# Kernel optimization log

Measured on AMD Instinct MI355X. Metric: run time of the kernel, lower is better.

The kernel has to match this reference:

```python
import jax, jax.numpy as jnp
import numpy as np

N_TRACKS = 2_000_000
N_EVENTS = 100_000
N_FEAT = 32
N_LATENT = 64


def setup_inputs() -> dict:
    key = jax.random.key(0)
    ks = jax.random.split(key, 12)
    x = jax.random.normal(ks[0], (N_TRACKS, N_FEAT), dtype=jnp.float32)
    # sorted event ids; guarantee every event id 0..N_EVENTS-1 appears so the
    # compacted segment count is exactly N_EVENTS (static shape under jit)
    extra = jax.random.randint(ks[1], (N_TRACKS - N_EVENTS,), 0, N_EVENTS)
    event_ids = jnp.sort(jnp.concatenate([jnp.arange(N_EVENTS), extra])).astype(jnp.int64)

    def lin(k, fan_in, fan_out):
        return jax.random.normal(k, (fan_in, fan_out), dtype=jnp.float32) / np.sqrt(fan_in)

    return {
        "x": x,
        "event_ids": event_ids,
        "phi_w1": lin(ks[2], N_FEAT, 2 * N_FEAT),
        "phi_b1": jnp.zeros((2 * N_FEAT,), jnp.float32),
        "phi_w2": lin(ks[3], 2 * N_FEAT, N_LATENT),
        "phi_b2": jnp.zeros((N_LATENT,), jnp.float32),
        "rho_w1": lin(ks[4], N_LATENT, 2 * N_LATENT),
        "rho_b1": jnp.zeros((2 * N_LATENT,), jnp.float32),
        "rho_w2": lin(ks[5], 2 * N_LATENT, N_LATENT),
        "rho_b2": jnp.zeros((N_LATENT,), jnp.float32),
        "rho_w3": lin(ks[6], N_LATENT, 1),
        "rho_b3": jnp.zeros((1,), jnp.float32),
    }


def reference(x, event_ids, phi_w1, phi_b1, phi_w2, phi_b2,
              rho_w1, rho_b1, rho_w2, rho_b2, rho_w3, rho_b3):
    # phi: per-track MLP  [N, F] -> [N, L]
    h = jax.nn.relu(x @ phi_w1 + phi_b1)
    h = jax.nn.relu(h @ phi_w2 + phi_b2)
    # compact segment ids from sorted event ids (cumsum of change flags)
    change = (event_ids[1:] != event_ids[:-1]).astype(jnp.int32)
    idxs = jnp.concatenate([jnp.zeros((1,), jnp.int32), jnp.cumsum(change)])
    # segment-sum pooling: [N, L] -> [E, L]
    pooled = jax.ops.segment_sum(h, idxs, num_segments=N_EVENTS)
    # rho: per-event MLP -> sigmoid scalar
    r = jax.nn.relu(pooled @ rho_w1 + rho_b1)
    r = jax.nn.relu(r @ rho_w2 + rho_b2)
    return jax.nn.sigmoid(r @ rho_w3 + rho_b3)
```

## Files before the change

kernel.cpp:

```cpp
#include <hip/hip_runtime.h>
#include <hip/hip_bf16.h>
#include <math.h>

#define N_FEAT 32
#define N_HID  64
#define N_LAT  64
#define R_HID  128
#define TILES_PER_WAVE 16
#define STREAM (4 * TILES_PER_WAVE)
#define H1W 88
#define R1W 136

typedef short s16x8 __attribute__((ext_vector_type(8)));
typedef short s16x4 __attribute__((ext_vector_type(4)));
typedef float f32x4 __attribute__((ext_vector_type(4)));
typedef int   i32x4 __attribute__((ext_vector_type(4)));

__device__ __forceinline__ short bfs(float f) {
    __bf16 b = (__bf16)f;
    return __builtin_bit_cast(short, b);
}
__device__ __forceinline__ float bff(short s) {
    return (float)__builtin_bit_cast(__bf16, s);
}
__device__ __forceinline__ f32x4 mfma16(s16x8 a, s16x8 b, f32x4 c) {
    return __builtin_amdgcn_mfma_f32_16x16x32_bf16(a, b, c, 0, 0, 0);
}
__device__ __forceinline__ void split8(f32x4 a, f32x4 b, s16x8& h, s16x8& l) {
    #pragma unroll
    for (int j = 0; j < 4; ++j) {
        short h0 = bfs(a[j]); h[j] = h0;     l[j] = bfs(a[j] - bff(h0));
        short h1 = bfs(b[j]); h[4 + j] = h1; l[4 + j] = bfs(b[j] - bff(h1));
    }
}
__device__ __forceinline__ s16x8 pack8(f32x4 a, f32x4 b) {
    s16x8 h;
    #pragma unroll
    for (int j = 0; j < 4; ++j) { h[j] = bfs(a[j]); h[4 + j] = bfs(b[j]); }
    return h;
}

__device__ __forceinline__ void load_bfrag(const float* __restrict__ w, int k0, int c,
                                           s16x8& hi, s16x8& lo) {
    #pragma unroll
    for (int j = 0; j < 8; ++j) {
        float f = w[(size_t)(k0 + j) * 64 + c];
        short h = bfs(f);
        hi[j] = h;
        lo[j] = bfs(f - bff(h));
    }
}

__global__ __launch_bounds__(256) void zero_kernel(f32x4* __restrict__ p, int n4)
{
    int i = blockIdx.x * blockDim.x + threadIdx.x;
    int stride = gridDim.x * blockDim.x;
    f32x4 z = {0.f, 0.f, 0.f, 0.f};
    for (; i < n4; i += stride) p[i] = z;
}

__global__ __launch_bounds__(256, 4) void phi_mfma_kernel(
    const float* __restrict__ x,
    const int*   __restrict__ eids,
    const float* __restrict__ w1, const float* __restrict__ b1,
    const float* __restrict__ w2, const float* __restrict__ b2,
    float* __restrict__ pooled, int n_tracks)
{
    __shared__ s16x8 wfrag[16][64];
    __shared__ short h1s[4][16 * H1W];

    const int lane = threadIdx.x & 63;
    const int wv   = threadIdx.x >> 6;
    const int g    = lane >> 4;
    const int r    = lane & 15;
    const int sg   = r >> 2;
    const int so   = r & 3;

    #pragma unroll
    for (int ff = 0; ff < 4; ++ff) {
        int f   = wv + 4 * ff;
        int idx = f & 7;
        int s   = idx >> 2;
        int n   = idx & 3;
        bool lo = (f >= 8);
        s16x8 v;
        #pragma unroll
        for (int j = 0; j < 8; ++j) {
            float fv = w2[(size_t)(32 * s + 8 * g + j) * 64 + (r + 16 * n)];
            short h  = bfs(fv);
            v[j] = lo ? bfs(fv - bff(h)) : h;
        }
        wfrag[f][lane] = v;
    }
    __syncthreads();

    short* h1w = h1s[wv];
    const long long wbase = ((long long)blockIdx.x * 4 + wv) * (4LL * STREAM);
    if (wbase >= n_tracks) return;

    s16x8 w1h[4], w1l[4];
    #pragma unroll
    for (int n = 0; n < 4; ++n) load_bfrag(w1, 8 * g, 4 * r + n, w1h[n], w1l[n]);

    float b1v[4], b2v[4];
    #pragma unroll
    for (int n = 0; n < 4; ++n) { b1v[n] = b1[4 * r + n]; b2v[n] = b2[r + 16 * n]; }

    #define LOADX(T, XA, XB) {                                                    \
        long long row_ = wbase + (long long)sg * STREAM + 4 * (T) + so;           \
        if (row_ > n_tracks - 1) row_ = n_tracks - 1;                             \
        XA = *(const f32x4*)(x + row_ * N_FEAT + 8 * g);                          \
        XB = *(const f32x4*)(x + row_ * N_FEAT + 8 * g + 4);                      \
    }
    #define LOADE(T, E4) {                                                        \
        long long ib_ = wbase + (long long)g * STREAM + 4 * (T);                  \
        if (ib_ > n_tracks - 4) ib_ = (n_tracks - 4) & ~3LL;                      \
        E4 = *(const i32x4*)(eids + ib_);                                         \
    }

    f32x4 xa, xb; i32x4 e4;
    LOADX(0, xa, xb)
    LOADE(0, e4)

    float carry[4] = {0.f, 0.f, 0.f, 0.f};
    int carry_id = -1;
    int dyn = 0;

    #pragma unroll 1
    for (int t = 0; t < TILES_PER_WAVE; ++t) {
        asm volatile("" : "+v"(dyn));
        const s16x8* wfl = (const s16x8*)&wfrag[0][lane] + dyn;

        long long tbg = wbase + (long long)g * STREAM + 4 * t;

        s16x8 xh = pack8(xa, xb);
        i32x4 e4c = e4;
        if (t + 1 < TILES_PER_WAVE) { LOADX(t + 1, xa, xb) LOADE(t + 1, e4) }

        f32x4 h1C[4];
        #pragma unroll
        for (int n = 0; n < 4; ++n) {
            f32x4 c = {0.f, 0.f, 0.f, 0.f};
            c = mfma16(xh, w1l[n], c);
            c = mfma16(xh, w1h[n], c);
            h1C[n] = c;
        }

        #pragma unroll
        for (int q = 0; q < 4; ++q) {
            s16x4 v;
            #pragma unroll
            for (int n = 0; n < 4; ++n)
                v[n] = bfs(fmaxf(h1C[n][q] + b1v[n], 0.f));
            *(s16x4*)&h1w[(4 * g + q) * H1W + 4 * r] = v;
        }

        s16x8 ah0 = *(const s16x8*)&h1w[r * H1W + 8 * g];
        s16x8 ah1 = *(const s16x8*)&h1w[r * H1W + 32 + 8 * g];

        f32x4 h2C[4] = {{0.f,0.f,0.f,0.f},{0.f,0.f,0.f,0.f},{0.f,0.f,0.f,0.f},{0.f,0.f,0.f,0.f}};
        #pragma unroll
        for (int n = 0; n < 4; ++n) {
            h2C[n] = mfma16(ah0, wfl[64 * (8 + n)], h2C[n]);
            h2C[n] = mfma16(ah0, wfl[64 * n],       h2C[n]);
            h2C[n] = mfma16(ah1, wfl[64 * (12 + n)], h2C[n]);
            h2C[n] = mfma16(ah1, wfl[64 * (4 + n)],  h2C[n]);
        }

        int remg = (int)(n_tracks - tbg);
        remg = remg < 0 ? 0 : (remg > 4 ? 4 : remg);
        const bool newrun   = (e4c[0] != carry_id);
        const bool doflush0 = newrun && (carry_id >= 0);
        const bool q01 = (e4c[1] != e4c[0]);
        const bool q12 = (e4c[2] != e4c[1]);
        const bool q23 = (e4c[3] != e4c[2]);
        #pragma unroll
        for (int n = 0; n < 4; ++n) {
            f32x4 hv;
            #pragma unroll
            for (int q = 0; q < 4; ++q) {
                float fq = fmaxf(h2C[n][q] + b2v[n], 0.f);
                hv[q] = (q < remg) ? fq : 0.f;
            }
            float* pp = pooled + (size_t)(r + 16 * n);
            float c = carry[n];
            if (doflush0) atomicAdd(pp + (size_t)carry_id * N_LAT, c);
            if (newrun)   c = 0.f;
            c += hv[0];
            if (q01) { atomicAdd(pp + (size_t)e4c[0] * N_LAT, c); c = 0.f; }
            c += hv[1];
            if (q12) { atomicAdd(pp + (size_t)e4c[1] * N_LAT, c); c = 0.f; }
            c += hv[2];
            if (q23) { atomicAdd(pp + (size_t)e4c[2] * N_LAT, c); c = 0.f; }
            c += hv[3];
            carry[n] = c;
        }
        carry_id = e4c[3];
    }

    if (carry_id >= 0) {
        #pragma unroll
        for (int n = 0; n < 4; ++n)
            atomicAdd(pooled + (size_t)carry_id * N_LAT + r + 16 * n, carry[n]);
    }
    #undef LOADX
    #undef LOADE
}

__global__ __launch_bounds__(256, 3) void rho1_kernel(
    const float* __restrict__ pooled,
    const float* __restrict__ w1, const float* __restrict__ b1,
    short* __restrict__ r1g, int n_events)
{
    __shared__ s16x8 wf[32][64];
    __shared__ short st[4][16 * R1W];

    const int lane = threadIdx.x & 63;
    const int wv   = threadIdx.x >> 6;
    const int g    = lane >> 4;
    const int r    = lane & 15;

    #pragma unroll
    for (int ff = 0; ff < 8; ++ff) {
        int f = wv + 4 * ff;
        int plane = f >> 4;
        int idx = f & 15;
        int ks = idx >> 3, nt = idx & 7;
        s16x8 v;
        #pragma unroll
        for (int j = 0; j < 8; ++j) {
            float fv = w1[(size_t)(32 * ks + 8 * g + j) * R_HID + (r + 16 * nt)];
            short h  = bfs(fv);
            v[j] = plane ? bfs(fv - bff(h)) : h;
        }
        wf[f][lane] = v;
    }
    __syncthreads();

    const long long ebase = ((long long)blockIdx.x * 4 + wv) * 16;
    if (ebase >= n_events) return;

    long long prow = ebase + r; if (prow > n_events - 1) prow = n_events - 1;
    const f32x4* pr = (const f32x4*)(pooled + prow * N_LAT);
    s16x8 xh0, xl0, xh1, xl1;
    split8(pr[2 * g],     pr[2 * g + 1], xh0, xl0);
    split8(pr[8 + 2 * g], pr[9 + 2 * g], xh1, xl1);

    short* stw = st[wv];
    #pragma unroll
    for (int nt = 0; nt < 8; ++nt) {
        s16x8 wh0 = wf[nt][lane],      wl0 = wf[16 + nt][lane];
        s16x8 wh1 = wf[8 + nt][lane],  wl1 = wf[24 + nt][lane];
        f32x4 c = {0.f, 0.f, 0.f, 0.f};
        c = mfma16(xl0, wh0, c);
        c = mfma16(xh0, wl0, c);
        c = mfma16(xh0, wh0, c);
        c = mfma16(xl1, wh1, c);
        c = mfma16(xh1, wl1, c);
        c = mfma16(xh1, wh1, c);
        float bv = b1[r + 16 * nt];
        #pragma unroll
        for (int q = 0; q < 4; ++q)
            stw[(4 * g + q) * R1W + r + 16 * nt] = bfs(fmaxf(c[q] + bv, 0.f));
    }

    #pragma unroll
    for (int i = 0; i < 4; ++i) {
        int chunk = 64 * i + lane;
        int row = chunk >> 4;
        int off = (chunk & 15) * 8;
        s16x8 v = *(const s16x8*)&stw[row * R1W + off];
        long long er = ebase + row;
        if (er < n_events) *(s16x8*)(r1g + er * R_HID + off) = v;
    }
}

__global__ __launch_bounds__(256, 4) void rho2_kernel(
    const short* __restrict__ r1g,
    const float* __restrict__ w2, const float* __restrict__ b2,
    const float* __restrict__ w3, const float* __restrict__ b3,
    float* __restrict__ out, int n_events)
{
    __shared__ s16x8 wf[32][64];

    const int lane = threadIdx.x & 63;
    const int wv   = threadIdx.x >> 6;
    const int g    = lane >> 4;
    const int r    = lane & 15;

    #pragma unroll
    for (int ff = 0; ff < 8; ++ff) {
        int f = wv + 4 * ff;
        int plane = f >> 4;
        int idx = f & 15;
        int ks = idx >> 2, nt = idx & 3;
        s16x8 v;
        #pragma unroll
        for (int j = 0; j < 8; ++j) {
            float fv = w2[(size_t)(32 * ks + 8 * g + j) * N_LAT + (r + 16 * nt)];
            short h  = bfs(fv);
            v[j] = plane ? bfs(fv - bff(h)) : h;
        }
        wf[f][lane] = v;
    }
    __syncthreads();

    const long long ebase = ((long long)blockIdx.x * 4 + wv) * 16;
    if (ebase >= n_events) return;

    long long arow = ebase + r; if (arow > n_events - 1) arow = n_events - 1;
    s16x8 ah[4];
    #pragma unroll
    for (int ks = 0; ks < 4; ++ks)
        ah[ks] = *(const s16x8*)(r1g + arow * R_HID + 32 * ks + 8 * g);

    float s0 = 0.f, s1 = 0.f, s2 = 0.f, s3 = 0.f;
    #pragma unroll
    for (int nt = 0; nt < 4; ++nt) {
        f32x4 c = {0.f, 0.f, 0.f, 0.f};
        #pragma unroll
        for (int ks = 0; ks < 4; ++ks) {
            c = mfma16(ah[ks], wf[16 + ks * 4 + nt][lane], c);
            c = mfma16(ah[ks], wf[ks * 4 + nt][lane],      c);
        }
        float bv = b2[r + 16 * nt];
        float wv3 = w3[r + 16 * nt];
        s0 = fmaf(fmaxf(c[0] + bv, 0.f), wv3, s0);
        s1 = fmaf(fmaxf(c[1] + bv, 0.f), wv3, s1);
        s2 = fmaf(fmaxf(c[2] + bv, 0.f), wv3, s2);
        s3 = fmaf(fmaxf(c[3] + bv, 0.f), wv3, s3);
    }
    #pragma unroll
    for (int off = 1; off < 16; off <<= 1) {
        s0 += __shfl_xor(s0, off, 64);
        s1 += __shfl_xor(s1, off, 64);
        s2 += __shfl_xor(s2, off, 64);
        s3 += __shfl_xor(s3, off, 64);
    }
    if (r == 0) {
        float b3v = b3[0];
        float zs[4] = {s0, s1, s2, s3};
        #pragma unroll
        for (int q = 0; q < 4; ++q) {
            long long e = ebase + 4 * g + q;
            if (e < n_events) out[e] = 1.f / (1.f + expf(-(zs[q] + b3v)));
        }
    }
}

extern "C" void kernel_launch(void* const* d_in, const int* in_sizes, int n_in,
                              void* d_out, int out_size, void* d_ws, size_t ws_size,
                              hipStream_t stream) {
    const float* x      = (const float*)d_in[0];
    const int*   eids   = (const int*)  d_in[1];
    const float* phi_w1 = (const float*)d_in[2];
    const float* phi_b1 = (const float*)d_in[3];
    const float* phi_w2 = (const float*)d_in[4];
    const float* phi_b2 = (const float*)d_in[5];
    const float* rho_w1 = (const float*)d_in[6];
    const float* rho_b1 = (const float*)d_in[7];
    const float* rho_w2 = (const float*)d_in[8];
    const float* rho_b2 = (const float*)d_in[9];
    const float* rho_w3 = (const float*)d_in[10];
    const float* rho_b3 = (const float*)d_in[11];
    float* out = (float*)d_out;

    int n_tracks = in_sizes[1];
    int n_events = out_size;

    float* pooled = (float*)d_ws;
    short* r1g    = (short*)((char*)d_ws +
                    (size_t)n_events * N_LAT * sizeof(float));

    int n4 = n_events * N_LAT / 4;
    zero_kernel<<<2048, 256, 0, stream>>>((f32x4*)pooled, n4);

    long long tracks_per_wave = 4LL * STREAM;
    long long waves  = ((long long)n_tracks + tracks_per_wave - 1) / tracks_per_wave;
    int phi_blocks   = (int)((waves + 3) / 4);
    phi_mfma_kernel<<<phi_blocks, 256, 0, stream>>>(
        x, eids, phi_w1, phi_b1, phi_w2, phi_b2, pooled, n_tracks);

    long long tiles = ((long long)n_events + 15) / 16;
    int rho_blocks = (int)((tiles + 3) / 4);
    rho1_kernel<<<rho_blocks, 256, 0, stream>>>(
        pooled, rho_w1, rho_b1, r1g, n_events);
    rho2_kernel<<<rho_blocks, 256, 0, stream>>>(
        r1g, rho_w2, rho_b2, rho_w3, rho_b3, out, n_events);
}
```

Before: 115.4 us.

## Fuse rho layers into one kernel and double-buffer phi input prefetch

Merges the two rho kernels into one that keeps the first-layer activations in shared memory rather than writing them to global and reading them back. The shared weight-fragment array is reused for the second-layer weights after a barrier. Separately, the phi kernel now prefetches input tiles two iterations ahead instead of one, to hide more load latency at the cost of extra registers. The fused kernel adds barriers and refills shared-memory weights inside every block, and the deeper prefetch may reduce occupancy in phi.

```diff
diff --git a/kernel.cpp b/kernel.cpp
--- a/kernel.cpp
+++ b/kernel.cpp
@@ -118,9 +118,9 @@
         E4 = *(const i32x4*)(eids + ib_);                                         \
     }
 
-    f32x4 xa, xb; i32x4 e4;
-    LOADX(0, xa, xb)
-    LOADE(0, e4)
+    f32x4 xaA, xbA, xaB, xbB; i32x4 e4A, e4B;
+    LOADX(0, xaA, xbA) LOADE(0, e4A)
+    LOADX(1, xaB, xbB) LOADE(1, e4B)
 
     float carry[4] = {0.f, 0.f, 0.f, 0.f};
     int carry_id = -1;
@@ -133,9 +133,10 @@
 
         long long tbg = wbase + (long long)g * STREAM + 4 * t;
 
-        s16x8 xh = pack8(xa, xb);
-        i32x4 e4c = e4;
-        if (t + 1 < TILES_PER_WAVE) { LOADX(t + 1, xa, xb) LOADE(t + 1, e4) }
+        s16x8 xh = pack8(xaA, xbA);
+        i32x4 e4c = e4A;
+        xaA = xaB; xbA = xbB; e4A = e4B;
+        if (t + 2 < TILES_PER_WAVE) { LOADX(t + 2, xaB, xbB) LOADE(t + 2, e4B) }
 
         f32x4 h1C[4];
         #pragma unroll
@@ -207,10 +208,12 @@
     #undef LOADE
 }
 
-__global__ __launch_bounds__(256, 3) void rho1_kernel(
+__global__ __launch_bounds__(256, 3) void rho_fused_kernel(
     const float* __restrict__ pooled,
     const float* __restrict__ w1, const float* __restrict__ b1,
-    short* __restrict__ r1g, int n_events)
+    const float* __restrict__ w2, const float* __restrict__ b2,
+    const float* __restrict__ w3, const float* __restrict__ b3,
+    float* __restrict__ out, int n_events)
 {
     __shared__ s16x8 wf[32][64];
     __shared__ short st[4][16 * R1W];
@@ -219,6 +222,9 @@
     const int wv   = threadIdx.x >> 6;
     const int g    = lane >> 4;
     const int r    = lane & 15;
+
+    const long long ebase = ((long long)blockIdx.x * 4 + wv) * 16;
+    const bool active = (ebase < n_events);
 
     #pragma unroll
     for (int ff = 0; ff < 8; ++ff) {
@@ -237,56 +243,32 @@
     }
     __syncthreads();
 
-    const long long ebase = ((long long)blockIdx.x * 4 + wv) * 16;
-    if (ebase >= n_events) return;
-
-    long long prow = ebase + r; if (prow > n_events - 1) prow = n_events - 1;
-    const f32x4* pr = (const f32x4*)(pooled + prow * N_LAT);
-    s16x8 xh0, xl0, xh1, xl1;
-    split8(pr[2 * g],     pr[2 * g + 1], xh0, xl0);
-    split8(pr[8 + 2 * g], pr[9 + 2 * g], xh1, xl1);
-
     short* stw = st[wv];
-    #pragma unroll
-    for (int nt = 0; nt < 8; ++nt) {
-        s16x8 wh0 = wf[nt][lane],      wl0 = wf[16 + nt][lane];
-        s16x8 wh1 = wf[8 + nt][lane],  wl1 = wf[24 + nt][lane];
-        f32x4 c = {0.f, 0.f, 0.f, 0.f};
-        c = mfma16(xl0, wh0, c);
-        c = mfma16(xh0, wl0, c);
-        c = mfma16(xh0, wh0, c);
-        c = mfma16(xl1, wh1, c);
-        c = mfma16(xh1, wl1, c);
-        c = mfma16(xh1, wh1, c);
-        float bv = b1[r + 16 * nt];
-        #pragma unroll
-        for (int q = 0; q < 4; ++q)
-            stw[(4 * g + q) * R1W + r + 16 * nt] = bfs(fmaxf(c[q] + bv, 0.f));
-    }
-
-    #pragma unroll
-    for (int i = 0; i < 4; ++i) {
-        int chunk = 64 * i + lane;
-        int row = chunk >> 4;
-        int off = (chunk & 15) * 8;
-        s16x8 v = *(const s16x8*)&stw[row * R1W + off];
-        long long er = ebase + row;
-        if (er < n_events) *(s16x8*)(r1g + er * R_HID + off) = v;
-    }
-}
-
-__global__ __launch_bounds__(256, 4) void rho2_kernel(
-    const short* __restrict__ r1g,
-    const float* __restrict__ w2, const float* __restrict__ b2,
-    const float* __restrict__ w3, const float* __restrict__ b3,
-    float* __restrict__ out, int n_events)
-{
-    __shared__ s16x8 wf[32][64];
-
-    const int lane = threadIdx.x & 63;
-    const int wv   = threadIdx.x >> 6;
-    const int g    = lane >> 4;
-    const int r    = lane & 15;
+    if (active) {
+        long long prow = ebase + r; if (prow > n_events - 1) prow = n_events - 1;
+        const f32x4* pr = (const f32x4*)(pooled + prow * N_LAT);
+        s16x8 xh0, xl0, xh1, xl1;
+        split8(pr[2 * g],     pr[2 * g + 1], xh0, xl0);
+        split8(pr[8 + 2 * g], pr[9 + 2 * g], xh1, xl1);
+
+        #pragma unroll
+        for (int nt = 0; nt < 8; ++nt) {
+            s16x8 wh0 = wf[nt][lane],      wl0 = wf[16 + nt][lane];
+            s16x8 wh1 = wf[8 + nt][lane],  wl1 = wf[24 + nt][lane];
+            f32x4 c = {0.f, 0.f, 0.f, 0.f};
+            c = mfma16(xl0, wh0, c);
+            c = mfma16(xh0, wl0, c);
+            c = mfma16(xh0, wh0, c);
+            c = mfma16(xl1, wh1, c);
+            c = mfma16(xh1, wl1, c);
+            c = mfma16(xh1, wh1, c);
+            float bv = b1[r + 16 * nt];
+            #pragma unroll
+            for (int q = 0; q < 4; ++q)
+                stw[(4 * g + q) * R1W + r + 16 * nt] = bfs(fmaxf(c[q] + bv, 0.f));
+        }
+    }
+    __syncthreads();
 
     #pragma unroll
     for (int ff = 0; ff < 8; ++ff) {
@@ -305,14 +287,12 @@
     }
     __syncthreads();
 
-    const long long ebase = ((long long)blockIdx.x * 4 + wv) * 16;
-    if (ebase >= n_events) return;
-
-    long long arow = ebase + r; if (arow > n_events - 1) arow = n_events - 1;
+    if (!active) return;
+
     s16x8 ah[4];
     #pragma unroll
     for (int ks = 0; ks < 4; ++ks)
-        ah[ks] = *(const s16x8*)(r1g + arow * R_HID + 32 * ks + 8 * g);
+        ah[ks] = *(const s16x8*)&stw[r * R1W + 32 * ks + 8 * g];
 
     float s0 = 0.f, s1 = 0.f, s2 = 0.f, s3 = 0.f;
     #pragma unroll
@@ -369,8 +349,6 @@
     int n_events = out_size;
 
     float* pooled = (float*)d_ws;
-    short* r1g    = (short*)((char*)d_ws +
-                    (size_t)n_events * N_LAT * sizeof(float));
 
     int n4 = n_events * N_LAT / 4;
     zero_kernel<<<2048, 256, 0, stream>>>((f32x4*)pooled, n4);
@@ -383,8 +361,6 @@
 
     long long tiles = ((long long)n_events + 15) / 16;
     int rho_blocks = (int)((tiles + 3) / 4);
-    rho1_kernel<<<rho_blocks, 256, 0, stream>>>(
-        pooled, rho_w1, rho_b1, r1g, n_events);
-    rho2_kernel<<<rho_blocks, 256, 0, stream>>>(
-        r1g, rho_w2, rho_b2, rho_w3, rho_b3, out, n_events);
-}
+    rho_fused_kernel<<<rho_blocks, 256, 0, stream>>>(
+        pooled, rho_w1, rho_b1, rho_w2, rho_b2, rho_w3, rho_b3, out, n_events);
+}
```

Result: no change. 114.5 us (-0.8%).
